# Optimization experiments

Hardware: AMD Instinct MI355X
Metric: run time of the kernel (lower is better)

## Reference

```python
import jax, jax.numpy as jnp
import numpy as np

B = 262144
STATE_DIM = 12
ACTION_DIM = 1
MSG_DIM = 32
MAX_CHILDREN = 2
EPS = 1e-12  # F.normalize default eps


def _l2norm(x):
    n = jnp.sqrt(jnp.sum(x * x, axis=-1, keepdims=True))
    return x / jnp.maximum(n, EPS)


def setup_inputs() -> dict:
    key = jax.random.key(0)
    ks = jax.random.split(key, 16)

    def lin(kw, kb, out_d, in_d):
        lim = 1.0 / np.sqrt(in_d)
        w = jax.random.uniform(kw, (out_d, in_d), jnp.float32, -lim, lim)
        b = jax.random.uniform(kb, (out_d,), jnp.float32, -lim, lim)
        return w, b

    state = jax.random.normal(ks[0], (B, STATE_DIM), jnp.float32)
    action = jax.random.normal(ks[1], (B, ACTION_DIM), jnp.float32)

    # ModelUp (sNet): fc1, fc2, fc3
    up_w1, up_b1 = lin(ks[2], ks[3], 64, STATE_DIM + ACTION_DIM)
    up_w2, up_b2 = lin(ks[4], ks[5], 64, 64 + MSG_DIM * MAX_CHILDREN)
    up_w3, up_b3 = lin(ks[6], ks[7], MSG_DIM, 64)

    # ModelDownAction.model = MLPBase(msg_dim + action_dim + msg_dim, msg_dim)
    dyn_w1, dyn_b1 = lin(ks[8], ks[9], 400, MSG_DIM + ACTION_DIM + MSG_DIM)
    dyn_w2, dyn_b2 = lin(ks[10], ks[11], 300, 400)
    dyn_w3, dyn_b3 = lin(ks[12], ks[13], MSG_DIM, 300)

    return dict(state=state, action=action,
                up_w1=up_w1, up_b1=up_b1, up_w2=up_w2, up_b2=up_b2,
                up_w3=up_w3, up_b3=up_b3,
                dyn_w1=dyn_w1, dyn_b1=dyn_b1, dyn_w2=dyn_w2, dyn_b2=dyn_b2,
                dyn_w3=dyn_w3, dyn_b3=dyn_b3)


def reference(state, action,
              up_w1, up_b1, up_w2, up_b2, up_w3, up_b3,
              dyn_w1, dyn_b1, dyn_w2, dyn_b2, dyn_w3, dyn_b3):
    # num_limbs == 1, parents = [-1], td = bu = True, disable_fold = True
    x = state                              # (B, state_dim)
    u = action                             # (B, 1)

    # ---- bottom_up_transmission(0): ModelUp with all-zero child messages ----
    m_children = jnp.zeros((B, MSG_DIM * MAX_CHILDREN), x.dtype)
    xu = jnp.concatenate([x, u], axis=-1)
    xu = _l2norm(xu @ up_w1.T + up_b1)                       # (B, 64)
    xum = jnp.tanh(jnp.concatenate([xu, m_children], axis=-1))
    xum = jnp.tanh(xum @ up_w2.T + up_b2)                    # (B, 64)
    msg_up = _l2norm(xum @ up_w3.T + up_b3)                  # (B, msg_dim)

    # ---- top_down_transmission(0): ModelDownAction, state := msg_up ----
    # parent_msg = zeros, self_children_idx = 0 -> msg_in = zeros slice
    msg_in = jnp.zeros((B, MSG_DIM), x.dtype)
    xum2 = jnp.concatenate([msg_up, u, msg_in], axis=-1)     # (B, 2*msg_dim+1)
    h = jax.nn.relu(xum2 @ dyn_w1.T + dyn_b1)                # (B, 400)
    h = jax.nn.relu(h @ dyn_w2.T + dyn_b2)                   # (B, 300)
    delta = h @ dyn_w3.T + dyn_b3                            # (B, msg_dim)

    # stack over num_limbs=1 then squeeze -> (B, msg_dim)
    return delta
```

## Files before the change

kernel.cpp:

```cpp
#include <hip/hip_runtime.h>
#include <stdint.h>

typedef short s16x8 __attribute__((ext_vector_type(8)));
typedef float f32x16 __attribute__((ext_vector_type(16)));
typedef unsigned int u32;
typedef unsigned int u32x2 __attribute__((ext_vector_type(2)));

#define NFRAG 336
#define WS_USHORTS (NFRAG*512)
#define PANEL_FRAGS 24
#define PANEL_BYTES (PANEL_FRAGS*1024)
#define LDS_BYTES (2*PANEL_BYTES)

#define MFMA(a,b,c) __builtin_amdgcn_mfma_f32_32x32x16_bf16((a),(b),(c),0,0,0)

__device__ __forceinline__ unsigned short f2bf(float f){
  u32 x = __builtin_bit_cast(u32, f);
  x += 0x7fffu + ((x >> 16) & 1u);
  return (unsigned short)(x >> 16);
}

__device__ __forceinline__ float bfhi(float b){
  return __builtin_bit_cast(float, (u32)f2bf(b) << 16);
}

__device__ __forceinline__ u32 pkbf(float a, float b){
  u32 r;
  asm("v_cvt_pk_bf16_f32 %0, %1, %2" : "=v"(r) : "v"(a), "v"(b));
  return r;
}

__device__ __forceinline__ float fast_tanh(float x){
  float ax = fabsf(x);
  float e = __expf(-2.0f * ax);
  float r = (1.0f - e) * __builtin_amdgcn_rcpf(1.0f + e);
  return x < 0.0f ? -r : r;
}

__device__ __forceinline__ float halfsum(float s){
  return s + __shfl_xor(s, 32);
}

__device__ __forceinline__ void tile2frags(const f32x16 v, s16x8& f0, s16x8& f1){
  u32 w00 = pkbf(v[0],  v[1]),  w01 = pkbf(v[2],  v[3]);
  u32 w10 = pkbf(v[4],  v[5]),  w11 = pkbf(v[6],  v[7]);
  u32 w20 = pkbf(v[8],  v[9]),  w21 = pkbf(v[10], v[11]);
  u32 w30 = pkbf(v[12], v[13]), w31 = pkbf(v[14], v[15]);
  u32x2 p0 = __builtin_amdgcn_permlane32_swap(w00, w10, false, false);
  u32x2 p1 = __builtin_amdgcn_permlane32_swap(w01, w11, false, false);
  u32x2 p2 = __builtin_amdgcn_permlane32_swap(w20, w30, false, false);
  u32x2 p3 = __builtin_amdgcn_permlane32_swap(w21, w31, false, false);
  int4 r0, r1;
  r0.x = (int)p0[0]; r0.y = (int)p1[0]; r0.z = (int)p0[1]; r0.w = (int)p1[1];
  r1.x = (int)p2[0]; r1.y = (int)p3[0]; r1.z = (int)p2[1]; r1.w = (int)p3[1];
  f0 = __builtin_bit_cast(s16x8, r0);
  f1 = __builtin_bit_cast(s16x8, r1);
}

__global__ void wconv_kernel(const float* __restrict__ uw1, const float* __restrict__ ub1,
                             const float* __restrict__ uw2, const float* __restrict__ ub2,
                             const float* __restrict__ uw3, const float* __restrict__ ub3,
                             const float* __restrict__ dw1, const float* __restrict__ db1,
                             const float* __restrict__ dw2, const float* __restrict__ db2,
                             const float* __restrict__ dw3, const float* __restrict__ db3,
                             unsigned short* __restrict__ wp)
{
  int i = blockIdx.x*256 + threadIdx.x;
  if (i >= WS_USHORTS) return;
  int f    = i >> 9;
  int lane = (i >> 3) & 63;
  int j    = i & 7;
  int row  = lane & 31;
  int k8   = (lane >> 5)*8 + j;
  float v = 0.0f;
  if (f < 2){
    int feat = f*32 + row; int k = k8;
    if (k < 13) v = uw1[feat*13 + k];
    else if (k == 13) v = ub1[feat];
    else if (k == 14) v = ub1[feat] - bfhi(ub1[feat]);
  } else if (f < 12){
    int t = f - 2; int kt = t >> 1, nt = t & 1;
    int feat = nt*32 + row; int k = kt*16 + k8;
    if (k < 64) v = uw2[feat*128 + k];
    else if (k == 64) v = ub2[feat];
    else if (k == 65) v = ub2[feat] - bfhi(ub2[feat]);
  } else if (f < 17){
    int kt = f - 12; int feat = row; int k = kt*16 + k8;
    if (k < 64) v = uw3[feat*64 + k];
    else if (k == 64) v = ub3[feat];
    else if (k == 65) v = ub3[feat] - bfhi(ub3[feat]);
  } else if (f < 56){
    int t = f - 17; int nt = t/3, kt = t%3;
    int feat = nt*32 + row; int k = kt*16 + k8;
    if (feat < 400){
      if (k < 33) v = dw1[feat*65 + k];
      else if (k == 33) v = db1[feat];
      else if (k == 34) v = db1[feat] - bfhi(db1[feat]);
    } else if ((feat == 400 || feat == 401) && k == 33) v = 1.0f;
  } else {
    int t = f - 56; int n = t/56; int r = t%56;
    if (r < 52){
      int kf = r >> 1, nt = r & 1;
      int feat = n*64 + nt*32 + row; int k = kf*16 + k8;
      if (feat < 300){
        if (k < 400) v = dw2[feat*400 + k];
        else if (k == 400) v = db2[feat];
        else if (k == 401) v = db2[feat] - bfhi(db2[feat]);
      } else if ((feat == 300 || feat == 301) && k == 400) v = 1.0f;
    } else {
      int kt = n*4 + (r - 52); int feat = row; int k = kt*16 + k8;
      if (k < 300) v = dw3[feat*300 + k];
      else if (k == 300) v = db3[feat];
      else if (k == 301) v = db3[feat] - bfhi(db3[feat]);
    }
  }
  wp[i] = f2bf(v);
}

__device__ __forceinline__ s16x8 fragF(const char* sm, int f, int ln){
  return *(const s16x8*)(sm + ((f/PANEL_FRAGS) & 1)*PANEL_BYTES
                            + (f % PANEL_FRAGS)*1024 + ln*16);
}

__device__ __forceinline__ void stage24(const unsigned short* wp, char* sm, int panel, int tid){
  char* dst = sm + (panel & 1)*PANEL_BYTES;
  const char* src = (const char*)wp + (size_t)panel*PANEL_BYTES;
  #pragma unroll
  for (int j = 0; j < 6; ++j){
    int off = j*4096 + tid*16;
    __builtin_amdgcn_global_load_lds(
      (const __attribute__((address_space(1))) unsigned int*)(src + off),
      (__attribute__((address_space(3))) unsigned int*)(dst + off), 16, 0, 0);
  }
}

#define BND(NP) { __syncthreads(); if ((NP) <= 13) stage24(wp, sm, (NP), tid); }

#define D1TRIPLE(f0_, oA, oB) { \
  f32x16 a = {}; \
  __builtin_amdgcn_s_setprio(1); \
  a = MFMA(fragF(sm, (f0_)+0, ln), mf0, a); \
  a = MFMA(fragF(sm, (f0_)+1, ln), mf1, a); \
  a = MFMA(fragF(sm, (f0_)+2, ln), mf2, a); \
  __builtin_amdgcn_s_setprio(0); \
  _Pragma("unroll") \
  for (int r = 0; r < 16; ++r) a[r] = fmaxf(a[r], 0.f); \
  tile2frags(a, oA, oB); }

#define D2RUN(fb, r0, r1) { \
  __builtin_amdgcn_s_setprio(1); \
  _Pragma("unroll") \
  for (int r = (r0); r < (r1); ++r){ \
    s16x8 hb = h1f[r>>1]; \
    if (r & 1) d2a1 = MFMA(fragF(sm, (fb)+r, ln), hb, d2a1); \
    else       d2a0 = MFMA(fragF(sm, (fb)+r, ln), hb, d2a0); \
  } \
  __builtin_amdgcn_s_setprio(0); }

#define D2TAIL(fb) { \
  _Pragma("unroll") \
  for (int r = 0; r < 16; ++r){ \
    d2a0[r] = fmaxf(d2a0[r], 0.f); \
    d2a1[r] = fmaxf(d2a1[r], 0.f); \
  } \
  s16x8 c0, c1, c2, c3; \
  tile2frags(d2a0, c0, c1); \
  tile2frags(d2a1, c2, c3); \
  __builtin_amdgcn_s_setprio(1); \
  acc3 = MFMA(fragF(sm, (fb)+52, ln), c0, acc3); \
  acc3 = MFMA(fragF(sm, (fb)+53, ln), c1, acc3); \
  acc3 = MFMA(fragF(sm, (fb)+54, ln), c2, acc3); \
  acc3 = MFMA(fragF(sm, (fb)+55, ln), c3, acc3); \
  __builtin_amdgcn_s_setprio(0); }

__global__ __launch_bounds__(256, 2) void fused_kernel(
    const float* __restrict__ state, const float* __restrict__ action,
    const unsigned short* __restrict__ wp, float* __restrict__ out)
{
  __shared__ __align__(1024) char sm[LDS_BYTES];

  const int tid = threadIdx.x;
  const int ln  = tid & 63;
  const int wid = tid >> 6;
  const int c   = ln & 31;
  const int h   = ln >> 5;
  const int rowb = blockIdx.x*128 + wid*32;

  const float* xr = state + (size_t)(rowb + c)*12;
  float u = action[rowb + c];
  float4 xa, xb;
  if (h == 0){
    xa = *(const float4*)xr;
    xb = *(const float4*)(xr + 4);
  } else {
    xa = *(const float4*)(xr + 8);
    xb = float4{u, 1.0f, 1.0f, 0.0f};
  }

  stage24(wp, sm, 0, tid);
  __syncthreads();
  stage24(wp, sm, 1, tid);

  int4 xw;
  xw.x = pkbf(xa.x, xa.y); xw.y = pkbf(xa.z, xa.w);
  xw.z = pkbf(xb.x, xb.y); xw.w = pkbf(xb.z, xb.w);
  s16x8 xfrag = __builtin_bit_cast(s16x8, xw);
  int4 ow = {0,0,0,0}; if (h == 0) ow.x = 0x3F803F80;
  s16x8 onef = __builtin_bit_cast(s16x8, ow);
  int4 mw = {0,0,0,0};
  if (h == 0){ mw.x = pkbf(u, 1.0f); mw.y = 0x3F80; }
  s16x8 mf2 = __builtin_bit_cast(s16x8, mw);

  s16x8 mf0, mf1;
  {
    s16x8 xf0, xf1, xf2, xf3, tf0, tf1, tf2, tf3;
    {
      f32x16 a0 = {}, a1 = {};
      a0 = MFMA(fragF(sm, 0, ln), xfrag, a0);
      a1 = MFMA(fragF(sm, 1, ln), xfrag, a1);
      float s = 0.f;
      #pragma unroll
      for (int r = 0; r < 16; ++r) s += a0[r]*a0[r] + a1[r]*a1[r];
      s = halfsum(s);
      float inv = __builtin_amdgcn_rsqf(fmaxf(s, 1e-24f));
      #pragma unroll
      for (int r = 0; r < 16; ++r){
        a0[r] = fast_tanh(a0[r]*inv);
        a1[r] = fast_tanh(a1[r]*inv);
      }
      tile2frags(a0, xf0, xf1);
      tile2frags(a1, xf2, xf3);
    }
    {
      f32x16 a0 = {}, a1 = {};
      __builtin_amdgcn_s_setprio(1);
      a0 = MFMA(fragF(sm, 2, ln), xf0, a0);  a1 = MFMA(fragF(sm, 3, ln), xf0, a1);
      a0 = MFMA(fragF(sm, 4, ln), xf1, a0);  a1 = MFMA(fragF(sm, 5, ln), xf1, a1);
      a0 = MFMA(fragF(sm, 6, ln), xf2, a0);  a1 = MFMA(fragF(sm, 7, ln), xf2, a1);
      a0 = MFMA(fragF(sm, 8, ln), xf3, a0);  a1 = MFMA(fragF(sm, 9, ln), xf3, a1);
      a0 = MFMA(fragF(sm,10, ln), onef, a0); a1 = MFMA(fragF(sm,11, ln), onef, a1);
      __builtin_amdgcn_s_setprio(0);
      #pragma unroll
      for (int r = 0; r < 16; ++r){
        a0[r] = fast_tanh(a0[r]);
        a1[r] = fast_tanh(a1[r]);
      }
      tile2frags(a0, tf0, tf1);
      tile2frags(a1, tf2, tf3);
    }
    {
      f32x16 m = {};
      __builtin_amdgcn_s_setprio(1);
      m = MFMA(fragF(sm,12, ln), tf0, m);
      m = MFMA(fragF(sm,13, ln), tf1, m);
      m = MFMA(fragF(sm,14, ln), tf2, m);
      m = MFMA(fragF(sm,15, ln), tf3, m);
      m = MFMA(fragF(sm,16, ln), onef, m);
      __builtin_amdgcn_s_setprio(0);
      float s = 0.f;
      #pragma unroll
      for (int r = 0; r < 16; ++r) s += m[r]*m[r];
      s = halfsum(s);
      float inv = __builtin_amdgcn_rsqf(fmaxf(s, 1e-24f));
      #pragma unroll
      for (int r = 0; r < 16; ++r) m[r] *= inv;
      tile2frags(m, mf0, mf1);
    }
  }

  s16x8 h1f[26];
  D1TRIPLE(17, h1f[0],  h1f[1])
  D1TRIPLE(20, h1f[2],  h1f[3])
  {
    f32x16 a = {};
    __builtin_amdgcn_s_setprio(1);
    a = MFMA(fragF(sm, 23, ln), mf0, a);
    __builtin_amdgcn_s_setprio(0);
    BND(2)
    __builtin_amdgcn_s_setprio(1);
    a = MFMA(fragF(sm, 24, ln), mf1, a);
    a = MFMA(fragF(sm, 25, ln), mf2, a);
    __builtin_amdgcn_s_setprio(0);
    #pragma unroll
    for (int r = 0; r < 16; ++r) a[r] = fmaxf(a[r], 0.f);
    tile2frags(a, h1f[4], h1f[5]);
  }
  D1TRIPLE(26, h1f[6],  h1f[7])
  D1TRIPLE(29, h1f[8],  h1f[9])
  D1TRIPLE(32, h1f[10], h1f[11])
  D1TRIPLE(35, h1f[12], h1f[13])
  D1TRIPLE(38, h1f[14], h1f[15])
  D1TRIPLE(41, h1f[16], h1f[17])
  D1TRIPLE(44, h1f[18], h1f[19])
  {
    f32x16 a = {};
    __builtin_amdgcn_s_setprio(1);
    a = MFMA(fragF(sm, 47, ln), mf0, a);
    __builtin_amdgcn_s_setprio(0);
    BND(3)
    __builtin_amdgcn_s_setprio(1);
    a = MFMA(fragF(sm, 48, ln), mf1, a);
    a = MFMA(fragF(sm, 49, ln), mf2, a);
    __builtin_amdgcn_s_setprio(0);
    #pragma unroll
    for (int r = 0; r < 16; ++r) a[r] = fmaxf(a[r], 0.f);
    tile2frags(a, h1f[20], h1f[21]);
  }
  D1TRIPLE(50, h1f[22], h1f[23])
  D1TRIPLE(53, h1f[24], h1f[25])

  f32x16 acc3 = {};
  {
    f32x16 d2a0 = {}, d2a1 = {};
    D2RUN(56, 0, 16)
    BND(4)
    D2RUN(56, 16, 40)
    BND(5)
    D2RUN(56, 40, 52)
    D2TAIL(56)
  }
  {
    f32x16 d2a0 = {}, d2a1 = {};
    D2RUN(112, 0, 8)
    BND(6)
    D2RUN(112, 8, 32)
    BND(7)
    D2RUN(112, 32, 52)
    D2TAIL(112)
  }
  {
    f32x16 d2a0 = {}, d2a1 = {};
    BND(8)
    D2RUN(168, 0, 24)
    BND(9)
    D2RUN(168, 24, 48)
    BND(10)
    D2RUN(168, 48, 52)
    D2TAIL(168)
  }
  {
    f32x16 d2a0 = {}, d2a1 = {};
    D2RUN(224, 0, 16)
    BND(11)
    D2RUN(224, 16, 40)
    BND(12)
    D2RUN(224, 40, 52)
    D2TAIL(224)
  }
  {
    f32x16 d2a0 = {}, d2a1 = {};
    D2RUN(280, 0, 8)
    BND(13)
    D2RUN(280, 8, 32)
    BND(14)
    D2RUN(280, 32, 52)
    D2TAIL(280)
  }

  float* op = out + (size_t)(rowb + c)*32;
  #pragma unroll
  for (int p = 0; p < 4; ++p){
    float4 v4 = {acc3[4*p+0], acc3[4*p+1], acc3[4*p+2], acc3[4*p+3]};
    *(float4*)(op + p*8 + h*4) = v4;
  }
}

extern "C" void kernel_launch(void* const* d_in, const int* in_sizes, int n_in,
                              void* d_out, int out_size, void* d_ws, size_t ws_size,
                              hipStream_t stream)
{
  const float* state  = (const float*)d_in[0];
  const float* action = (const float*)d_in[1];
  const float* up_w1  = (const float*)d_in[2];
  const float* up_b1  = (const float*)d_in[3];
  const float* up_w2  = (const float*)d_in[4];
  const float* up_b2  = (const float*)d_in[5];
  const float* up_w3  = (const float*)d_in[6];
  const float* up_b3  = (const float*)d_in[7];
  const float* dyn_w1 = (const float*)d_in[8];
  const float* dyn_b1 = (const float*)d_in[9];
  const float* dyn_w2 = (const float*)d_in[10];
  const float* dyn_b2 = (const float*)d_in[11];
  const float* dyn_w3 = (const float*)d_in[12];
  const float* dyn_b3 = (const float*)d_in[13];
  unsigned short* wp = (unsigned short*)d_ws;

  hipLaunchKernelGGL(wconv_kernel, dim3((WS_USHORTS + 255)/256), dim3(256), 0, stream,
                     up_w1, up_b1, up_w2, up_b2, up_w3, up_b3,
                     dyn_w1, dyn_b1, dyn_w2, dyn_b2, dyn_w3, dyn_b3, wp);
  hipLaunchKernelGGL(fused_kernel, dim3(262144/128), dim3(256), 0, stream,
                     state, action, wp, (float*)d_out);
}
```

Before: 93.63 us.

## Switch weight staging to triple-buffered 14-fragment panels with partial vmcnt waits

Weight panels shrink from 24 to 14 fragments and LDS holds three of them instead of two. Each panel is now prefetched two steps ahead. __syncthreads is replaced by an explicit s_waitcnt vmcnt(4) plus s_barrier, so the newest panel's loads can stay in flight while the previous one is consumed. This aims to hide global-to-LDS latency behind MFMA work, at the cost of more barriers (24 vs ~14) and slightly less LDS per block.

```diff
diff --git a/kernel.cpp b/kernel.cpp
--- a/kernel.cpp
+++ b/kernel.cpp
@@ -8,9 +8,9 @@
 
 #define NFRAG 336
 #define WS_USHORTS (NFRAG*512)
-#define PANEL_FRAGS 24
+#define PANEL_FRAGS 14
 #define PANEL_BYTES (PANEL_FRAGS*1024)
-#define LDS_BYTES (2*PANEL_BYTES)
+#define LDS_BYTES (3*PANEL_BYTES)
 
 #define MFMA(a,b,c) __builtin_amdgcn_mfma_f32_32x32x16_bf16((a),(b),(c),0,0,0)
 
@@ -118,23 +118,33 @@
 }
 
 __device__ __forceinline__ s16x8 fragF(const char* sm, int f, int ln){
-  return *(const s16x8*)(sm + ((f/PANEL_FRAGS) & 1)*PANEL_BYTES
+  return *(const s16x8*)(sm + ((f/PANEL_FRAGS) % 3)*PANEL_BYTES
                             + (f % PANEL_FRAGS)*1024 + ln*16);
 }
 
-__device__ __forceinline__ void stage24(const unsigned short* wp, char* sm, int panel, int tid){
-  char* dst = sm + (panel & 1)*PANEL_BYTES;
+__device__ __forceinline__ void stage14(const unsigned short* wp, char* sm, int panel, int tid){
+  char* dst = sm + (panel % 3)*PANEL_BYTES;
   const char* src = (const char*)wp + (size_t)panel*PANEL_BYTES;
   #pragma unroll
-  for (int j = 0; j < 6; ++j){
+  for (int j = 0; j < 3; ++j){
     int off = j*4096 + tid*16;
     __builtin_amdgcn_global_load_lds(
       (const __attribute__((address_space(1))) unsigned int*)(src + off),
       (__attribute__((address_space(3))) unsigned int*)(dst + off), 16, 0, 0);
   }
-}
-
-#define BND(NP) { __syncthreads(); if ((NP) <= 13) stage24(wp, sm, (NP), tid); }
+  int off3 = 12288 + (tid & 127)*16;
+  __builtin_amdgcn_global_load_lds(
+    (const __attribute__((address_space(1))) unsigned int*)(src + off3),
+    (__attribute__((address_space(3))) unsigned int*)(dst + off3), 16, 0, 0);
+}
+
+#define BND(P) { \
+  if ((P) >= 23) { asm volatile("s_waitcnt vmcnt(0) lgkmcnt(0)" ::: "memory"); } \
+  else           { asm volatile("s_waitcnt vmcnt(4) lgkmcnt(0)" ::: "memory"); } \
+  __builtin_amdgcn_s_barrier(); \
+  __builtin_amdgcn_sched_barrier(0); \
+  if ((P)+2 <= 23) stage14(wp, sm, (P)+2, tid); \
+}
 
 #define D1TRIPLE(f0_, oA, oB) { \
   f32x16 a = {}; \
@@ -173,6 +183,19 @@
   acc3 = MFMA(fragF(sm, (fb)+55, ln), c3, acc3); \
   __builtin_amdgcn_s_setprio(0); }
 
+#define CHUNK(fb, P0) { \
+  f32x16 d2a0 = {}, d2a1 = {}; \
+  BND(P0) \
+  D2RUN(fb, 0, 14) \
+  BND((P0)+1) \
+  D2RUN(fb, 14, 28) \
+  BND((P0)+2) \
+  D2RUN(fb, 28, 42) \
+  BND((P0)+3) \
+  D2RUN(fb, 42, 52) \
+  D2TAIL(fb) \
+}
+
 __global__ __launch_bounds__(256, 2) void fused_kernel(
     const float* __restrict__ state, const float* __restrict__ action,
     const unsigned short* __restrict__ wp, float* __restrict__ out)
@@ -188,19 +211,19 @@
 
   const float* xr = state + (size_t)(rowb + c)*12;
   float u = action[rowb + c];
-  float4 xa, xb;
+  float4 xa, xbr;
   if (h == 0){
-    xa = *(const float4*)xr;
-    xb = *(const float4*)(xr + 4);
+    xa  = *(const float4*)xr;
+    xbr = *(const float4*)(xr + 4);
   } else {
-    xa = *(const float4*)(xr + 8);
-    xb = float4{u, 1.0f, 1.0f, 0.0f};
-  }
-
-  stage24(wp, sm, 0, tid);
-  __syncthreads();
-  stage24(wp, sm, 1, tid);
-
+    xa  = *(const float4*)(xr + 8);
+  }
+
+  stage14(wp, sm, 0, tid);
+  stage14(wp, sm, 1, tid);
+  BND(0)
+
+  float4 xb = (h == 0) ? xbr : float4{u, 1.0f, 1.0f, 0.0f};
   int4 xw;
   xw.x = pkbf(xa.x, xa.y); xw.y = pkbf(xa.z, xa.w);
   xw.z = pkbf(xb.x, xb.y); xw.w = pkbf(xb.z, xb.w);
@@ -253,6 +276,9 @@
       __builtin_amdgcn_s_setprio(1);
       m = MFMA(fragF(sm,12, ln), tf0, m);
       m = MFMA(fragF(sm,13, ln), tf1, m);
+      __builtin_amdgcn_s_setprio(0);
+      BND(1)
+      __builtin_amdgcn_s_setprio(1);
       m = MFMA(fragF(sm,14, ln), tf2, m);
       m = MFMA(fragF(sm,15, ln), tf3, m);
       m = MFMA(fragF(sm,16, ln), onef, m);
@@ -271,91 +297,50 @@
   s16x8 h1f[26];
   D1TRIPLE(17, h1f[0],  h1f[1])
   D1TRIPLE(20, h1f[2],  h1f[3])
+  D1TRIPLE(23, h1f[4],  h1f[5])
   {
     f32x16 a = {};
     __builtin_amdgcn_s_setprio(1);
-    a = MFMA(fragF(sm, 23, ln), mf0, a);
+    a = MFMA(fragF(sm, 26, ln), mf0, a);
+    a = MFMA(fragF(sm, 27, ln), mf1, a);
     __builtin_amdgcn_s_setprio(0);
     BND(2)
     __builtin_amdgcn_s_setprio(1);
-    a = MFMA(fragF(sm, 24, ln), mf1, a);
-    a = MFMA(fragF(sm, 25, ln), mf2, a);
+    a = MFMA(fragF(sm, 28, ln), mf2, a);
     __builtin_amdgcn_s_setprio(0);
     #pragma unroll
     for (int r = 0; r < 16; ++r) a[r] = fmaxf(a[r], 0.f);
-    tile2frags(a, h1f[4], h1f[5]);
-  }
-  D1TRIPLE(26, h1f[6],  h1f[7])
+    tile2frags(a, h1f[6], h1f[7]);
+  }
   D1TRIPLE(29, h1f[8],  h1f[9])
   D1TRIPLE(32, h1f[10], h1f[11])
   D1TRIPLE(35, h1f[12], h1f[13])
   D1TRIPLE(38, h1f[14], h1f[15])
-  D1TRIPLE(41, h1f[16], h1f[17])
-  D1TRIPLE(44, h1f[18], h1f[19])
   {
     f32x16 a = {};
     __builtin_amdgcn_s_setprio(1);
-    a = MFMA(fragF(sm, 47, ln), mf0, a);
+    a = MFMA(fragF(sm, 41, ln), mf0, a);
     __builtin_amdgcn_s_setprio(0);
     BND(3)
     __builtin_amdgcn_s_setprio(1);
-    a = MFMA(fragF(sm, 48, ln), mf1, a);
-    a = MFMA(fragF(sm, 49, ln), mf2, a);
+    a = MFMA(fragF(sm, 42, ln), mf1, a);
+    a = MFMA(fragF(sm, 43, ln), mf2, a);
     __builtin_amdgcn_s_setprio(0);
     #pragma unroll
     for (int r = 0; r < 16; ++r) a[r] = fmaxf(a[r], 0.f);
-    tile2frags(a, h1f[20], h1f[21]);
-  }
+    tile2frags(a, h1f[16], h1f[17]);
+  }
+  D1TRIPLE(44, h1f[18], h1f[19])
+  D1TRIPLE(47, h1f[20], h1f[21])
   D1TRIPLE(50, h1f[22], h1f[23])
   D1TRIPLE(53, h1f[24], h1f[25])
 
   f32x16 acc3 = {};
-  {
-    f32x16 d2a0 = {}, d2a1 = {};
-    D2RUN(56, 0, 16)
-    BND(4)
-    D2RUN(56, 16, 40)
-    BND(5)
-    D2RUN(56, 40, 52)
-    D2TAIL(56)
-  }
-  {
-    f32x16 d2a0 = {}, d2a1 = {};
-    D2RUN(112, 0, 8)
-    BND(6)
-    D2RUN(112, 8, 32)
-    BND(7)
-    D2RUN(112, 32, 52)
-    D2TAIL(112)
-  }
-  {
-    f32x16 d2a0 = {}, d2a1 = {};
-    BND(8)
-    D2RUN(168, 0, 24)
-    BND(9)
-    D2RUN(168, 24, 48)
-    BND(10)
-    D2RUN(168, 48, 52)
-    D2TAIL(168)
-  }
-  {
-    f32x16 d2a0 = {}, d2a1 = {};
-    D2RUN(224, 0, 16)
-    BND(11)
-    D2RUN(224, 16, 40)
-    BND(12)
-    D2RUN(224, 40, 52)
-    D2TAIL(224)
-  }
-  {
-    f32x16 d2a0 = {}, d2a1 = {};
-    D2RUN(280, 0, 8)
-    BND(13)
-    D2RUN(280, 8, 32)
-    BND(14)
-    D2RUN(280, 32, 52)
-    D2TAIL(280)
-  }
+  CHUNK(56,  4)
+  CHUNK(112, 8)
+  CHUNK(168, 12)
+  CHUNK(224, 16)
+  CHUNK(280, 20)
 
   float* op = out + (size_t)(rowb + c)*32;
   #pragma unroll
```

Result: no change. 94.16 us (+0.6%).
